# Optimization experiments

Measured on AMD Instinct MI355X. Metric: run time of the kernel, lower is better.

The kernel has to match this reference:

```python
import jax, jax.numpy as jnp
import numpy as np

NUM_IM = 2
NUM_OBJS = 64
NUM_PAIRS = 256
C = 512          # mid_dim == backbone channels
H = 28
W = 28
POOL = 7
STRIDE = 16.0
NUM_RELS = 51
PDIM = 4096
FLAT = C * POOL * POOL  # 25088


def _lin(key, out_d, in_d):
    return jax.random.normal(key, (out_d, in_d), jnp.float32) / np.sqrt(in_d)


def setup_inputs() -> dict:
    key = jax.random.key(0)
    ks = jax.random.split(key, 16)
    fmaps = jax.random.normal(ks[0], (NUM_IM, C, H, W), jnp.float32)
    reduce_obj_feats = jax.random.normal(ks[1], (NUM_OBJS, C), jnp.float32)
    # rois: [im_ind, x1, y1, x2, y2] in image pixel coords (image ~ 448 px)
    im_col = (jnp.arange(NUM_OBJS) % NUM_IM).astype(jnp.float32)
    pts = jax.random.uniform(ks[2], (NUM_OBJS, 2, 2), jnp.float32, 0.0, 447.0)
    lo = jnp.min(pts, axis=1)  # [N,2] -> x1,y1
    hi = jnp.max(pts, axis=1) + 8.0
    rois = jnp.concatenate([im_col[:, None], lo[:, 0:1], lo[:, 1:2],
                            jnp.clip(hi[:, 0:1], 0, 447), jnp.clip(hi[:, 1:2], 0, 447)], axis=1)
    so = jax.random.randint(ks[3], (NUM_PAIRS, 2), 0, NUM_OBJS)
    rel_inds = jnp.concatenate([jnp.zeros((NUM_PAIRS, 1), jnp.int32), so.astype(jnp.int32)], axis=1)
    params = dict(
        w_dw=_lin(ks[4], C * 9, C), b_dw=jnp.zeros((C * 9,), jnp.float32),
        w_pw=_lin(ks[5], C * C, C), b_pw=jnp.zeros((C * C,), jnp.float32),
        w_red=_lin(ks[6], C, C), b_red=jnp.zeros((C,), jnp.float32),
        w_rec=_lin(ks[7], C, 2 * C), b_rec=jnp.zeros((C,), jnp.float32),
        w_fc1=_lin(ks[8], PDIM, FLAT), b_fc1=jnp.zeros((PDIM,), jnp.float32),
        w_fc2=_lin(ks[9], PDIM, PDIM), b_fc2=jnp.zeros((PDIM,), jnp.float32),
        w_rel=_lin(ks[10], NUM_RELS, PDIM), b_rel=jnp.zeros((NUM_RELS,), jnp.float32),
    )
    return dict(fmaps=fmaps, rois=rois, rel_inds=rel_inds,
                reduce_obj_feats=reduce_obj_feats, **params)


def _roi_align(fmap, box):
    # fmap: [C,H,W]; box: [x1,y1,x2,y2] image coords. 7x7 bilinear sampling.
    b = box / STRIDE
    grid = (jnp.arange(POOL, dtype=jnp.float32) + 0.5) / POOL
    xs = jnp.clip(b[0] + grid * (b[2] - b[0]), 0.0, W - 1.0)
    ys = jnp.clip(b[1] + grid * (b[3] - b[1]), 0.0, H - 1.0)
    y0 = jnp.floor(ys).astype(jnp.int32); x0 = jnp.floor(xs).astype(jnp.int32)
    y1 = jnp.minimum(y0 + 1, H - 1);      x1 = jnp.minimum(x0 + 1, W - 1)
    wy = (ys - y0.astype(ys.dtype))[:, None]
    wx = (xs - x0.astype(xs.dtype))[None, :]
    f00 = fmap[:, y0[:, None], x0[None, :]]
    f01 = fmap[:, y0[:, None], x1[None, :]]
    f10 = fmap[:, y1[:, None], x0[None, :]]
    f11 = fmap[:, y1[:, None], x1[None, :]]
    return (f00 * (1 - wy) * (1 - wx) + f01 * (1 - wy) * wx
            + f10 * wy * (1 - wx) + f11 * wy * wx)  # [C,7,7]


def _forward(fmaps, rois, rel_inds, reduce_obj_feats,
             w_dw, b_dw, w_pw, b_pw, w_red, b_red, w_rec, b_rec,
             w_fc1, b_fc1, w_fc2, b_fc2, w_rel, b_rel):
    n = reduce_obj_feats.shape[0]
    im_inds = rois[:, 0].astype(jnp.int32)
    # per-object dynamic filters (gen-Linear bias folds into filter values)
    filt_dw = (reduce_obj_feats @ w_dw.T + b_dw).reshape(n, C, 3, 3)
    filt_pw = (reduce_obj_feats @ w_pw.T + b_pw).reshape(n, C, C)  # [N, Cout, Cin]
    red = jax.nn.relu(jnp.einsum('bchw,dc->bdhw', fmaps, w_red) + b_red[None, :, None, None])
    ext = red[im_inds]  # [N,C,H,W]
    # per-object depthwise 3x3, padding=1: 9 shifted multiply-adds
    xp = jnp.pad(ext, ((0, 0), (0, 0), (1, 1), (1, 1)))
    fd = jnp.zeros_like(ext)
    for i in range(3):
        for j in range(3):
            fd = fd + xp[:, :, i:i + H, j:j + W] * filt_dw[:, :, i, j][:, :, None, None]
    # per-object pointwise 1x1 (grouped conv with groups=num_objs)
    fp = jax.nn.relu(jnp.einsum('nchw,ndc->ndhw', fd, filt_pw))
    boxes = rois[:, 1:]
    sub = rel_inds[:, 1]
    obj = rel_inds[:, 2]
    s_fm = jax.vmap(_roi_align)(fp[sub], boxes[sub])  # [P,C,7,7]
    o_fm = jax.vmap(_roi_align)(fp[obj], boxes[obj])
    so = jnp.concatenate([s_fm, o_fm], axis=1)        # [P,2C,7,7]
    rec = jnp.einsum('pchw,dc->pdhw', so, w_rec) + b_rec[None, :, None, None]
    x = rec.reshape(rec.shape[0], -1)                  # Flattener
    x = jax.nn.relu(x @ w_fc1.T + b_fc1)               # VGG classifier (no dropout, no final relu)
    x = x @ w_fc2.T + b_fc2
    return x @ w_rel.T + b_rel                         # rel_compress


def reference(fmaps, rois, rel_inds, reduce_obj_feats,
              w_dw, b_dw, w_pw, b_pw, w_red, b_red, w_rec, b_rec,
              w_fc1, b_fc1, w_fc2, b_fc2, w_rel, b_rel):
    return _forward(fmaps, rois, rel_inds, reduce_obj_feats,
                    w_dw, b_dw, w_pw, b_pw, w_red, b_red, w_rec, b_rec,
                    w_fc1, b_fc1, w_fc2, b_fc2, w_rel, b_rel)
```

## Files before the change

kernel.cpp:

```cpp
#include <hip/hip_runtime.h>
#include <hip/hip_bf16.h>


namespace {
constexpr int NIM  = 2;
constexpr int NOBJ = 64;
constexpr int NPAIR= 256;
constexpr int CCH  = 512;
constexpr int H = 28, W = 28, HW = 784;
constexpr int PP = 49;
constexpr int NREL = 51;
constexpr int PDIM = 4096;
constexpr int FLAT = CCH * PP;

constexpr long OFF_FMT = 0;
constexpr long OFF_RED = OFF_FMT + (long)NIM * HW * CCH;
constexpr long OFF_FDW = OFF_RED + (long)NIM * HW * CCH;
constexpr long OFF_FPW = OFF_FDW + (long)NOBJ * CCH * 9;
constexpr long OFF_FD  = OFF_FPW + (long)NOBJ * CCH * CCH;
constexpr long OFF_FP  = OFF_FD  + (long)NOBJ * HW * CCH;
constexpr long OFF_X1  = OFF_FP  + (long)NOBJ * HW * CCH;
constexpr long OFF_X2  = OFF_X1  + (long)NPAIR * PDIM;
constexpr long OFF_SO  = OFF_FPW;
constexpr long OFF_X0  = OFF_FD;
constexpr long OFF_PART= OFF_FP;
}

typedef short bf16x8 __attribute__((ext_vector_type(8)));
typedef float f32x4  __attribute__((ext_vector_type(4)));

__global__ void transpose_k(const float* __restrict__ in, float* __restrict__ out) {
    __shared__ float tile[32][33];
    const int b  = blockIdx.z;
    const int p0 = blockIdx.x * 32, c0 = blockIdx.y * 32;
    const int tx = threadIdx.x, ty = threadIdx.y;
    int p = p0 + tx, c = c0 + ty;
    if (p < HW && c < CCH) tile[ty][tx] = in[((long)b * CCH + c) * HW + p];
    __syncthreads();
    int p2 = p0 + ty, c2 = c0 + tx;
    if (p2 < HW && c2 < CCH) out[((long)b * HW + p2) * CCH + c2] = tile[tx][ty];
}

template<bool RELU, bool TROUT, bool HAS_BIAS>
__global__ __launch_bounds__(256)
void gemm_nt64(const float* __restrict__ A, const float* __restrict__ B,
               const float* __restrict__ bias, float* __restrict__ C,
               int M, int N, int K, long sA, long sB, long sC) {
    constexpr int BM = 64, BN = 64, BK = 16;
    __shared__ float As[BK][BM];
    __shared__ float Bs[BK][BN];
    A += (long)blockIdx.z * sA;
    B += (long)blockIdx.z * sB;
    C += (long)blockIdx.z * sC;
    const int m0 = blockIdx.x * BM;
    const int n0 = blockIdx.y * BN;
    const int tid  = threadIdx.x;
    const int lrow = tid >> 2;
    const int lk4  = (tid & 3) << 2;
    const int tm   = (tid & 15) << 2;
    const int tn   = (tid >> 4) << 2;
    const int gma = m0 + lrow;
    const int gnb = n0 + lrow;
    const bool am = (gma < M);
    const bool bn = (gnb < N);
    const float* Ald = A + (long)gma * K + lk4;
    const float* Bld = B + (long)gnb * K + lk4;
    float acc[4][4] = {};
    for (int k0 = 0; k0 < K; k0 += BK) {
        float4 av = make_float4(0.f, 0.f, 0.f, 0.f);
        float4 bv = make_float4(0.f, 0.f, 0.f, 0.f);
        if (am) av = *(const float4*)(Ald + k0);
        if (bn) bv = *(const float4*)(Bld + k0);
        As[lk4 + 0][lrow] = av.x; As[lk4 + 1][lrow] = av.y;
        As[lk4 + 2][lrow] = av.z; As[lk4 + 3][lrow] = av.w;
        Bs[lk4 + 0][lrow] = bv.x; Bs[lk4 + 1][lrow] = bv.y;
        Bs[lk4 + 2][lrow] = bv.z; Bs[lk4 + 3][lrow] = bv.w;
        __syncthreads();
        #pragma unroll
        for (int kk = 0; kk < BK; ++kk) {
            float a[4], b[4];
            #pragma unroll
            for (int i = 0; i < 4; ++i) a[i] = As[kk][tm + i];
            #pragma unroll
            for (int j = 0; j < 4; ++j) b[j] = Bs[kk][tn + j];
            #pragma unroll
            for (int i = 0; i < 4; ++i)
                #pragma unroll
                for (int j = 0; j < 4; ++j)
                    acc[i][j] = fmaf(a[i], b[j], acc[i][j]);
        }
        __syncthreads();
    }
    #pragma unroll
    for (int i = 0; i < 4; ++i) {
        const int m = m0 + tm + i;
        if (m >= M) continue;
        #pragma unroll
        for (int j = 0; j < 4; ++j) {
            const int n = n0 + tn + j;
            if (n >= N) continue;
            float v = acc[i][j];
            if (HAS_BIAS) v += bias[n];
            if (RELU) v = fmaxf(v, 0.f);
            if (TROUT) C[(long)n * M + m] = v;
            else       C[(long)m * N + n] = v;
        }
    }
}

__device__ __forceinline__ void split_store(unsigned short* hp, unsigned short* lp,
                                            float4 v) {
    float f[4] = {v.x, v.y, v.z, v.w};
    ushort4 hv, lv;
    unsigned short h[4], l[4];
    #pragma unroll
    for (int t = 0; t < 4; ++t) {
        unsigned u = __float_as_uint(f[t]);
        h[t] = (unsigned short)(u >> 16);
        float hf = __uint_as_float((unsigned)h[t] << 16);
        l[t] = (unsigned short)(__float_as_uint(f[t] - hf) >> 16);
    }
    hv.x = h[0]; hv.y = h[1]; hv.z = h[2]; hv.w = h[3];
    lv.x = l[0]; lv.y = l[1]; lv.z = l[2]; lv.w = l[3];
    *(ushort4*)hp = hv;
    *(ushort4*)lp = lv;
}

template<bool RELU, bool HAS_BIAS>
__global__ __launch_bounds__(256)
void gemm_nt_mfma(const float* __restrict__ A, const float* __restrict__ B,
                  const float* __restrict__ bias, float* __restrict__ C,
                  int M, int N, int Kext, int lda, int ldb,
                  long sA, long sB, long sC) {
    constexpr int BM = 128, BN = 128, BK = 32;
    constexpr int PAD = 40;
    __shared__ unsigned short Ah[BM][PAD], Al[BM][PAD];
    __shared__ unsigned short Bh[BN][PAD], Bl[BN][PAD];
    A += (long)blockIdx.z * sA;
    B += (long)blockIdx.z * sB;
    C += (long)blockIdx.z * sC;
    const int m0 = blockIdx.x * BM, n0 = blockIdx.y * BN;
    const int tid  = threadIdx.x;
    const int lane = tid & 63;
    const int wid  = tid >> 6;
    const int wm = (wid >> 1) * 64, wn = (wid & 1) * 64;
    const int fr = lane & 15;
    const int k8 = (lane >> 4) * 8;
    f32x4 zero4 = {0.f, 0.f, 0.f, 0.f};
    f32x4 acc[4][4];
    #pragma unroll
    for (int i = 0; i < 4; ++i)
        #pragma unroll
        for (int j = 0; j < 4; ++j) acc[i][j] = zero4;

    for (int k0 = 0; k0 < Kext; k0 += BK) {
        #pragma unroll
        for (int i = 0; i < 4; ++i) {
            const int idx = tid + i * 256;
            const int r = idx >> 3;
            const int c = (idx & 7) << 2;
            float4 av = make_float4(0.f, 0.f, 0.f, 0.f);
            float4 bv = make_float4(0.f, 0.f, 0.f, 0.f);
            if (m0 + r < M) av = *(const float4*)(A + (long)(m0 + r) * lda + k0 + c);
            if (n0 + r < N) bv = *(const float4*)(B + (long)(n0 + r) * ldb + k0 + c);
            split_store(&Ah[r][c], &Al[r][c], av);
            split_store(&Bh[r][c], &Bl[r][c], bv);
        }
        __syncthreads();
        bf16x8 ah[4], al[4], bh[4], bl[4];
        #pragma unroll
        for (int f = 0; f < 4; ++f) {
            ah[f] = *(const bf16x8*)&Ah[wm + f * 16 + fr][k8];
            al[f] = *(const bf16x8*)&Al[wm + f * 16 + fr][k8];
            bh[f] = *(const bf16x8*)&Bh[wn + f * 16 + fr][k8];
            bl[f] = *(const bf16x8*)&Bl[wn + f * 16 + fr][k8];
        }
        #pragma unroll
        for (int i = 0; i < 4; ++i)
            #pragma unroll
            for (int j = 0; j < 4; ++j) {
                acc[i][j] = __builtin_amdgcn_mfma_f32_16x16x32_bf16(ah[i], bh[j], acc[i][j], 0, 0, 0);
                acc[i][j] = __builtin_amdgcn_mfma_f32_16x16x32_bf16(ah[i], bl[j], acc[i][j], 0, 0, 0);
                acc[i][j] = __builtin_amdgcn_mfma_f32_16x16x32_bf16(al[i], bh[j], acc[i][j], 0, 0, 0);
            }
        __syncthreads();
    }
    const int rg = (lane >> 4) << 2;
    #pragma unroll
    for (int i = 0; i < 4; ++i)
        #pragma unroll
        for (int j = 0; j < 4; ++j) {
            const int n = n0 + wn + j * 16 + fr;
            if (n >= N) continue;
            #pragma unroll
            for (int t = 0; t < 4; ++t) {
                const int m = m0 + wm + i * 16 + rg + t;
                if (m >= M) continue;
                float v = acc[i][j][t];
                if (HAS_BIAS) v += bias[n];
                if (RELU) v = fmaxf(v, 0.f);
                C[(long)m * N + n] = v;
            }
        }
}

template<bool RELU>
__global__ __launch_bounds__(256)
void reduce_splitk(const float* __restrict__ part, const float* __restrict__ bias,
                   float* __restrict__ out, int MN, int nmask, int S) {
    const int i = blockIdx.x * 256 + threadIdx.x;
    if (i >= MN) return;
    float v = bias[i & nmask];
    for (int s = 0; s < S; ++s) v += part[(long)s * MN + i];
    out[i] = RELU ? fmaxf(v, 0.f) : v;
}

__global__ void dwconv_k(const float* __restrict__ red, const float* __restrict__ fdw,
                         const float* __restrict__ rois, float* __restrict__ fd) {
    const int c  = threadIdx.x;
    const int hw = blockIdx.x;
    const int n  = blockIdx.y;
    const int y = hw / W, x = hw % W;
    const int b = (int)rois[n * 5];
    const float* rb = red + (long)b * HW * CCH;
    const float* w  = fdw + (long)n * (CCH * 9) + c * 9;
    float acc = 0.f;
    #pragma unroll
    for (int i = 0; i < 3; ++i) {
        const int yy = y + i - 1;
        if (yy < 0 || yy >= H) continue;
        #pragma unroll
        for (int j = 0; j < 3; ++j) {
            const int xx = x + j - 1;
            if (xx < 0 || xx >= W) continue;
            acc = fmaf(rb[(yy * W + xx) * CCH + c], w[i * 3 + j], acc);
        }
    }
    fd[((long)n * HW + hw) * CCH + c] = acc;
}

__global__ void roialign_k(const float* __restrict__ fp, const float* __restrict__ rois,
                           const int* __restrict__ rel, float* __restrict__ so) {
    const int c    = threadIdx.x;
    const int cell = blockIdx.x;
    const int side = blockIdx.y;
    const int p    = blockIdx.z;
    const int o = rel[p * 3 + 1 + side];
    const float* box = rois + o * 5 + 1;
    const float b0 = box[0] / 16.f, b1 = box[1] / 16.f;
    const float b2 = box[2] / 16.f, b3 = box[3] / 16.f;
    const int py = cell / 7, px = cell % 7;
    const float gx = (px + 0.5f) / 7.f, gy = (py + 0.5f) / 7.f;
    float xs = b0 + gx * (b2 - b0);
    float ys = b1 + gy * (b3 - b1);
    xs = fminf(fmaxf(xs, 0.f), (float)(W - 1));
    ys = fminf(fmaxf(ys, 0.f), (float)(H - 1));
    const int x0 = (int)floorf(xs), y0 = (int)floorf(ys);
    const int x1 = min(x0 + 1, W - 1), y1 = min(y0 + 1, H - 1);
    const float wx = xs - (float)x0, wy = ys - (float)y0;
    const float* f = fp + (long)o * HW * CCH;
    const float f00 = f[(y0 * W + x0) * CCH + c];
    const float f01 = f[(y0 * W + x1) * CCH + c];
    const float f10 = f[(y1 * W + x0) * CCH + c];
    const float f11 = f[(y1 * W + x1) * CCH + c];
    const float v = f00 * (1.f - wy) * (1.f - wx) + f01 * (1.f - wy) * wx
                  + f10 * wy * (1.f - wx)         + f11 * wy * wx;
    so[((long)p * PP + cell) * (2 * CCH) + side * CCH + c] = v;
}

extern "C" void kernel_launch(void* const* d_in, const int* in_sizes, int n_in,
                              void* d_out, int out_size, void* d_ws, size_t ws_size,
                              hipStream_t stream) {
    const float* fmaps = (const float*)d_in[0];
    const float* rois  = (const float*)d_in[1];
    const int*   rel   = (const int*)  d_in[2];
    const float* feats = (const float*)d_in[3];
    const float* w_dw  = (const float*)d_in[4];
    const float* b_dw  = (const float*)d_in[5];
    const float* w_pw  = (const float*)d_in[6];
    const float* b_pw  = (const float*)d_in[7];
    const float* w_red = (const float*)d_in[8];
    const float* b_red = (const float*)d_in[9];
    const float* w_rec = (const float*)d_in[10];
    const float* b_rec = (const float*)d_in[11];
    const float* w_fc1 = (const float*)d_in[12];
    const float* b_fc1 = (const float*)d_in[13];
    const float* w_fc2 = (const float*)d_in[14];
    const float* b_fc2 = (const float*)d_in[15];
    const float* w_rel = (const float*)d_in[16];
    const float* b_rel = (const float*)d_in[17];

    float* ws  = (float*)d_ws;
    float* out = (float*)d_out;
    float* fmt = ws + OFF_FMT;
    float* red = ws + OFF_RED;
    float* fdw = ws + OFF_FDW;
    float* fpw = ws + OFF_FPW;
    float* fd  = ws + OFF_FD;
    float* fpb = ws + OFF_FP;
    float* so  = ws + OFF_SO;
    float* x0  = ws + OFF_X0;
    float* x1  = ws + OFF_X1;
    float* x2  = ws + OFF_X2;
    float* part= ws + OFF_PART;

    transpose_k<<<dim3(25, 16, 2), dim3(32, 32), 0, stream>>>(fmaps, fmt);

    gemm_nt64<true, false, true><<<dim3(13, 8, 2), 256, 0, stream>>>(
        fmt, w_red, b_red, red, HW, CCH, CCH, (long)HW * CCH, 0, (long)HW * CCH);

    gemm_nt64<false, false, true><<<dim3(1, 72, 1), 256, 0, stream>>>(
        feats, w_dw, b_dw, fdw, NOBJ, CCH * 9, CCH, 0, 0, 0);

    gemm_nt_mfma<false, true><<<dim3(1, 2048, 1), 256, 0, stream>>>(
        feats, w_pw, b_pw, fpw, NOBJ, CCH * CCH, CCH, CCH, CCH, 0, 0, 0);

    dwconv_k<<<dim3(HW, NOBJ), CCH, 0, stream>>>(red, fdw, rois, fd);

    gemm_nt_mfma<true, false><<<dim3(7, 4, NOBJ), 256, 0, stream>>>(
        fd, fpw, nullptr, fpb, HW, CCH, CCH, CCH, CCH,
        (long)HW * CCH, (long)CCH * CCH, (long)HW * CCH);

    roialign_k<<<dim3(PP, 2, NPAIR), CCH, 0, stream>>>(fpb, rois, rel, so);

    gemm_nt64<false, true, true><<<dim3(1, 8, NPAIR), 256, 0, stream>>>(
        so, w_rec, b_rec, x0, PP, CCH, 2 * CCH, (long)PP * 2 * CCH, 0, (long)FLAT);

    {
        const int S = 16, Kc = FLAT / S;
        gemm_nt_mfma<false, false><<<dim3(2, 32, S), 256, 0, stream>>>(
            x0, w_fc1, nullptr, part, NPAIR, PDIM, Kc, FLAT, FLAT,
            (long)Kc, (long)Kc, (long)NPAIR * PDIM);
        reduce_splitk<true><<<dim3((NPAIR * PDIM) / 256), 256, 0, stream>>>(
            part, b_fc1, x1, NPAIR * PDIM, PDIM - 1, S);
    }

    {
        const int S = 4, Kc = PDIM / S;
        gemm_nt_mfma<false, false><<<dim3(2, 32, S), 256, 0, stream>>>(
            x1, w_fc2, nullptr, part, NPAIR, PDIM, Kc, PDIM, PDIM,
            (long)Kc, (long)Kc, (long)NPAIR * PDIM);
        reduce_splitk<false><<<dim3((NPAIR * PDIM) / 256), 256, 0, stream>>>(
            part, b_fc2, x2, NPAIR * PDIM, PDIM - 1, S);
    }

    gemm_nt64<false, false, true><<<dim3(4, 1, 1), 256, 0, stream>>>(
        x2, w_rel, b_rel, out, NPAIR, NREL, PDIM, 0, 0, 0);
}
```

Measured before the change: 2.424 ms.

## Prefetch next K tile in MFMA GEMM, move rec conv to MFMA, tune split-K

The MFMA GEMM now loads the next K tile's global data into registers while the current tile is being computed, replacing the __syncthreads pairs with raw barriers and an LDS waitcnt. Launch bounds now ask for 3 blocks per CU. The rec 1x1 conv, previously a batched gemm_nt64, becomes one large MFMA GEMM over all pairs×positions, with a scatter epilogue that writes the flattened layout directly. fc2 split-K is raised from 4 to 8. The register prefetch raises register pressure, and the scatter epilogue writes with a stride, giving poorly coalesced stores.

```diff
diff --git a/kernel.cpp b/kernel.cpp
--- a/kernel.cpp
+++ b/kernel.cpp
@@ -126,8 +126,8 @@
     *(ushort4*)lp = lv;
 }
 
-template<bool RELU, bool HAS_BIAS>
-__global__ __launch_bounds__(256)
+template<bool RELU, bool HAS_BIAS, int OUTMODE>
+__global__ __launch_bounds__(256, 3)
 void gemm_nt_mfma(const float* __restrict__ A, const float* __restrict__ B,
                   const float* __restrict__ bias, float* __restrict__ C,
                   int M, int N, int Kext, int lda, int ldb,
@@ -146,27 +146,36 @@
     const int wm = (wid >> 1) * 64, wn = (wid & 1) * 64;
     const int fr = lane & 15;
     const int k8 = (lane >> 4) * 8;
-    f32x4 zero4 = {0.f, 0.f, 0.f, 0.f};
+    const int r0 = tid >> 3;
+    const int cc = (tid & 7) << 2;
+    const float4 f4z = make_float4(0.f, 0.f, 0.f, 0.f);
     f32x4 acc[4][4];
     #pragma unroll
     for (int i = 0; i < 4; ++i)
         #pragma unroll
-        for (int j = 0; j < 4; ++j) acc[i][j] = zero4;
-
-    for (int k0 = 0; k0 < Kext; k0 += BK) {
+        for (int j = 0; j < 4; ++j) acc[i][j] = f32x4{0.f, 0.f, 0.f, 0.f};
+
+    float4 nA[4], nB[4];
+    auto issue = [&](int k0) {
         #pragma unroll
         for (int i = 0; i < 4; ++i) {
-            const int idx = tid + i * 256;
-            const int r = idx >> 3;
-            const int c = (idx & 7) << 2;
-            float4 av = make_float4(0.f, 0.f, 0.f, 0.f);
-            float4 bv = make_float4(0.f, 0.f, 0.f, 0.f);
-            if (m0 + r < M) av = *(const float4*)(A + (long)(m0 + r) * lda + k0 + c);
-            if (n0 + r < N) bv = *(const float4*)(B + (long)(n0 + r) * ldb + k0 + c);
-            split_store(&Ah[r][c], &Al[r][c], av);
-            split_store(&Bh[r][c], &Bl[r][c], bv);
-        }
-        __syncthreads();
+            const int r = r0 + i * 32;
+            nA[i] = (m0 + r < M) ? *(const float4*)(A + (long)(m0 + r) * lda + k0 + cc) : f4z;
+            nB[i] = (n0 + r < N) ? *(const float4*)(B + (long)(n0 + r) * ldb + k0 + cc) : f4z;
+        }
+    };
+    issue(0);
+    const int niter = Kext / BK;
+    for (int t = 0; t < niter; ++t) {
+        #pragma unroll
+        for (int i = 0; i < 4; ++i) {
+            const int r = r0 + i * 32;
+            split_store(&Ah[r][cc], &Al[r][cc], nA[i]);
+            split_store(&Bh[r][cc], &Bl[r][cc], nB[i]);
+        }
+        if (t + 1 < niter) issue((t + 1) * BK);
+        asm volatile("s_waitcnt lgkmcnt(0)" ::: "memory");
+        __builtin_amdgcn_s_barrier();
         bf16x8 ah[4], al[4], bh[4], bl[4];
         #pragma unroll
         for (int f = 0; f < 4; ++f) {
@@ -183,7 +192,7 @@
                 acc[i][j] = __builtin_amdgcn_mfma_f32_16x16x32_bf16(ah[i], bl[j], acc[i][j], 0, 0, 0);
                 acc[i][j] = __builtin_amdgcn_mfma_f32_16x16x32_bf16(al[i], bh[j], acc[i][j], 0, 0, 0);
             }
-        __syncthreads();
+        __builtin_amdgcn_s_barrier();
     }
     const int rg = (lane >> 4) << 2;
     #pragma unroll
@@ -199,7 +208,12 @@
                 float v = acc[i][j][t];
                 if (HAS_BIAS) v += bias[n];
                 if (RELU) v = fmaxf(v, 0.f);
-                C[(long)m * N + n] = v;
+                if (OUTMODE == 0) {
+                    C[(long)m * N + n] = v;
+                } else {
+                    const int p = m / PP, hw = m - p * PP;
+                    C[(long)p * FLAT + (long)n * PP + hw] = v;
+                }
             }
         }
 }
@@ -312,23 +326,23 @@
     gemm_nt64<false, false, true><<<dim3(1, 72, 1), 256, 0, stream>>>(
         feats, w_dw, b_dw, fdw, NOBJ, CCH * 9, CCH, 0, 0, 0);
 
-    gemm_nt_mfma<false, true><<<dim3(1, 2048, 1), 256, 0, stream>>>(
+    gemm_nt_mfma<false, true, 0><<<dim3(1, 2048, 1), 256, 0, stream>>>(
         feats, w_pw, b_pw, fpw, NOBJ, CCH * CCH, CCH, CCH, CCH, 0, 0, 0);
 
     dwconv_k<<<dim3(HW, NOBJ), CCH, 0, stream>>>(red, fdw, rois, fd);
 
-    gemm_nt_mfma<true, false><<<dim3(7, 4, NOBJ), 256, 0, stream>>>(
+    gemm_nt_mfma<true, false, 0><<<dim3(7, 4, NOBJ), 256, 0, stream>>>(
         fd, fpw, nullptr, fpb, HW, CCH, CCH, CCH, CCH,
         (long)HW * CCH, (long)CCH * CCH, (long)HW * CCH);
 
     roialign_k<<<dim3(PP, 2, NPAIR), CCH, 0, stream>>>(fpb, rois, rel, so);
 
-    gemm_nt64<false, true, true><<<dim3(1, 8, NPAIR), 256, 0, stream>>>(
-        so, w_rec, b_rec, x0, PP, CCH, 2 * CCH, (long)PP * 2 * CCH, 0, (long)FLAT);
+    gemm_nt_mfma<false, true, 1><<<dim3(98, 4, 1), 256, 0, stream>>>(
+        so, w_rec, b_rec, x0, NPAIR * PP, CCH, 2 * CCH, 2 * CCH, 2 * CCH, 0, 0, 0);
 
     {
         const int S = 16, Kc = FLAT / S;
-        gemm_nt_mfma<false, false><<<dim3(2, 32, S), 256, 0, stream>>>(
+        gemm_nt_mfma<false, false, 0><<<dim3(2, 32, S), 256, 0, stream>>>(
             x0, w_fc1, nullptr, part, NPAIR, PDIM, Kc, FLAT, FLAT,
             (long)Kc, (long)Kc, (long)NPAIR * PDIM);
         reduce_splitk<true><<<dim3((NPAIR * PDIM) / 256), 256, 0, stream>>>(
@@ -336,8 +350,8 @@
     }
 
     {
-        const int S = 4, Kc = PDIM / S;
-        gemm_nt_mfma<false, false><<<dim3(2, 32, S), 256, 0, stream>>>(
+        const int S = 8, Kc = PDIM / S;
+        gemm_nt_mfma<false, false, 0><<<dim3(2, 32, S), 256, 0, stream>>>(
             x1, w_fc2, nullptr, part, NPAIR, PDIM, Kc, PDIM, PDIM,
             (long)Kc, (long)Kc, (long)NPAIR * PDIM);
         reduce_splitk<false><<<dim3((NPAIR * PDIM) / 256), 256, 0, stream>>>(
```

New measurement: 2.357 ms. -2.7%, faster.
